# Performance work log

Hardware: AMD Instinct MI355X
Metric: run time of the kernel (lower is better)

The kernel has to match this reference:

```python
import jax, jax.numpy as jnp
import numpy as np

B, T, N, K = 8, 1024, 64, 8


def _normalize_logprob(logmat, axis):
    # temperature = 1 in forward_backward
    norm = jax.scipy.special.logsumexp(logmat, axis=axis, keepdims=True)
    return logmat - norm, norm


def setup_inputs() -> dict:
    key = jax.random.key(0)
    k1, k2, k3 = jax.random.split(key, 3)
    log_a = jax.random.normal(k1, (B, T, N, K, K), dtype=jnp.float32)
    log_b = jax.random.normal(k2, (B, T, N, K), dtype=jnp.float32)
    logprob_z1 = jax.random.normal(k3, (N, K), dtype=jnp.float32)
    return {"log_a": log_a, "log_b": log_b, "logprob_z1": logprob_z1}


def reference(log_a, log_b, logprob_z1):
    # log_a: (B,T,N,K,K)  transition log-probs a[t][i,j] = p(z_t=i | z_{t-1}=j)
    # log_b: (B,T,N,K)    emission log-likelihoods
    # logprob_z1: (N,K)   initial state log-prob (Z_init parameter)
    b_tm = jnp.moveaxis(log_b, 1, 0)  # (T,B,N,K) time-major for scan
    a_tm = jnp.moveaxis(log_a, 1, 0)  # (T,B,N,K,K)

    # ---- forward recursion ----
    alpha0, norm0 = _normalize_logprob(logprob_z1[None] + log_b[:, 0], -1)  # (B,N,K),(B,N,1)

    def fstep(prev, xs):
        b_t, a_t = xs  # (B,N,K), (B,N,K,K)
        # alpha_t[i] = logsumexp_j( b_t[i] + a_t[i,j] + prev[j] )
        u = jax.scipy.special.logsumexp(
            b_t[..., :, None] + a_t + prev[..., None, :], axis=-1)
        alpha, nrm = _normalize_logprob(u, -1)
        return alpha, (alpha, nrm)

    _, (alphas, fnorms) = jax.lax.scan(fstep, alpha0, (b_tm[1:], a_tm[1:]))
    forward_probs = jnp.moveaxis(
        jnp.concatenate([alpha0[None], alphas], axis=0), 0, 1)  # (B,T,N,K)

    # ---- backward recursion ----
    betaT = jnp.zeros_like(alpha0)  # (B,N,K)

    def bstep(nxt, xs):
        b_tp1, a_tp1 = xs  # (B,N,K), (B,N,K,K)
        # beta_t[j] = logsumexp_i( nxt[i] + a_tp1[i,j] + b_tp1[i] )
        u = jax.scipy.special.logsumexp(
            nxt[..., :, None] + a_tp1 + b_tp1[..., :, None], axis=-2)
        beta, nrm = _normalize_logprob(u, -1)
        return beta, (beta, nrm)

    _, (betas, bnorms) = jax.lax.scan(
        bstep, betaT, (b_tm[1:], a_tm[1:]), reverse=True)
    backward_probs = jnp.moveaxis(
        jnp.concatenate([betas, betaT[None]], axis=0), 0, 1)  # (B,T,N,K)

    # ---- posteriors ----
    gamma1, _ = _normalize_logprob(forward_probs + backward_probs, -1)  # (B,T,N,K)

    # gamma2[t][i,j] ~ beta_t[i] + a_t[i,j] + b_t[i] + alpha_{t-1}[j], t >= 1
    g2u = (forward_probs[:, :-1, :, None, :]      # (B,T-1,N,1,K)
           + backward_probs[:, 1:, :, :, None]    # (B,T-1,N,K,1)
           + log_a[:, 1:]                         # (B,T-1,N,K,K)
           + log_b[:, 1:][..., None])             # (B,T-1,N,K,1)
    g2_norm = jax.scipy.special.logsumexp(g2u, axis=(-2, -1), keepdims=True)
    gamma2_unpad = g2u - g2_norm
    gamma2 = jnp.concatenate(
        [jnp.zeros_like(gamma2_unpad[:, :1]), gamma2_unpad], axis=1)  # (B,T,N,K,K)

    return forward_probs, backward_probs, gamma1, gamma2
```

## Files before the change

kernel.cpp:

```cpp
#include <hip/hip_runtime.h>

#define Tdim 1024
#define Ndim 64
#define FSZ (8 * 1024 * 64 * 8)

typedef unsigned uint2v __attribute__((ext_vector_type(2)));

#define DPPADD(v, ctrl) ((v) + __int_as_float(__builtin_amdgcn_update_dpp( \
    0, __float_as_int(v), ctrl, 0xF, 0xF, false)))

__device__ __forceinline__ float swap_add16(float v) {
  unsigned u = __float_as_uint(v);
  uint2v r = __builtin_amdgcn_permlane16_swap(u, u, false, false);
  return __uint_as_float(r[0]) + __uint_as_float(r[1]);
}
__device__ __forceinline__ float swap_add32(float v) {
  unsigned u = __float_as_uint(v);
  uint2v r = __builtin_amdgcn_permlane32_swap(u, u, false, false);
  return __uint_as_float(r[0]) + __uint_as_float(r[1]);
}

#define SUM_LO3(v) { v = DPPADD(v, 0xB1); v = DPPADD(v, 0x4E); v = DPPADD(v, 0x141); }
#define SUM_HI3(v) { v = DPPADD(v, 0x128); v = swap_add16(v); v = swap_add32(v); }


__device__ __forceinline__ void fwd_load(const float* __restrict__ a_base,
                                         const float* __restrict__ b_base,
                                         int t0, int lane, int tr, int x, int y,
                                         float (&ra)[16], float (&rb)[16]) {
#pragma unroll
  for (int s = 0; s < 16; ++s) {
    int t = t0 + s; if (t > Tdim - 1) t = Tdim - 1;
    ra[s] = a_base[(size_t)t * (Ndim * 64) + ((s & 1) ? tr : lane)];
    rb[s] = b_base[(size_t)t * (Ndim * 8) + ((s & 1) ? y : x)];
  }
}

__device__ __forceinline__ void fwd_compute(int t0, int x, int y,
                                            const float (&ra)[16], const float (&rb)[16],
                                            float& q, float& sc,
                                            float* __restrict__ f_base) {
#pragma unroll
  for (int s = 0; s < 16; ++s) {
    int t = t0 + s;
    if (t < Tdim) {
      int oidx = (s & 1) ? y : x;
      float v = __expf(ra[s]) * q;
      if (!(s & 1)) { SUM_LO3(v); } else { SUM_HI3(v); }
      float S = v * (__expf(rb[s]) * sc);
      q = S;
      float T = S;
      if (!(s & 1)) { SUM_HI3(T); } else { SUM_LO3(T); }
      sc = __builtin_amdgcn_rcpf(T);
      float la = __logf(S * sc);
      if ((((s & 1) ? x : y)) == 0) f_base[(size_t)t * (Ndim * 8) + oidx] = la;
    }
  }
}

__device__ __forceinline__ void bwd_load(const float* __restrict__ a_base,
                                         const float* __restrict__ b_base,
                                         int t0, int lane, int tr, int x, int y,
                                         float (&ra)[16], float (&rb)[16]) {
#pragma unroll
  for (int s = 0; s < 16; ++s) {
    int t = t0 - s; if (t < 0) t = 0;
    ra[s] = a_base[(size_t)t * (Ndim * 64) + ((s & 1) ? tr : lane)];
    int tb = t0 - 1 - s; if (tb < 0) tb = 0;
    rb[s] = b_base[(size_t)tb * (Ndim * 8) + ((s & 1) ? x : y)];
  }
}

__device__ __forceinline__ void bwd_compute(int t0, int x, int y,
                                            const float (&ra)[16], const float (&rb)[16],
                                            float& u, float& sc,
                                            float* __restrict__ bo) {
#pragma unroll
  for (int s = 0; s < 16; ++s) {
    int tau = t0 - s;
    if (tau >= 1) {
      float v = __expf(ra[s]) * u;
      if (!(s & 1)) { SUM_HI3(v); } else { SUM_LO3(v); }
      int oidx = (s & 1) ? x : y;
      float unew = (__expf(rb[s]) * sc) * v;
      float W = v;
      if (!(s & 1)) { SUM_LO3(W); } else { SUM_HI3(W); }
      float scn = __builtin_amdgcn_rcpf(W);
      float lb = __logf(v * scn);
      if ((((s & 1) ? y : x)) == 0) bo[(size_t)(tau - 1) * (Ndim * 8) + oidx] = lb;
      u = unew;
      sc = scn;
    }
  }
}

__global__ __launch_bounds__(64, 1) void chains_kernel(const float* __restrict__ A,
                                                       const float* __restrict__ Bm,
                                                       const float* __restrict__ Z1,
                                                       float* __restrict__ Fout,
                                                       float* __restrict__ Bout) {
  const int lane = threadIdx.x;
  const int x = lane >> 3, y = lane & 7;
  const int tr = (y << 3) | x;
  const int chain = blockIdx.x & 511;
  const int b = chain >> 6, n = chain & 63;
  const size_t cbase = ((size_t)b * Tdim) * Ndim + n;
  const float* a_base = A + cbase * 64;
  const float* b_base = Bm + cbase * 8;

  float ra0[16], ra1[16], rb0[16], rb1[16];

  if (blockIdx.x < 512) {
    float* f_base = Fout + cbase * 8;
    float v0 = Z1[n * 8 + y] + b_base[y];
    float q = __expf(v0);
    float T0 = q; SUM_LO3(T0);
    if (x == 0) f_base[y] = v0 - __logf(T0);
    float sc = __builtin_amdgcn_rcpf(T0);
    fwd_load(a_base, b_base, 1, lane, tr, x, y, ra0, rb0);
#pragma unroll 1
    for (int kk = 0; kk < 64; kk += 2) {
      fwd_load(a_base, b_base, 1 + (kk + 1) * 16, lane, tr, x, y, ra1, rb1);
      __builtin_amdgcn_sched_barrier(0);
      fwd_compute(1 + kk * 16, x, y, ra0, rb0, q, sc, f_base);
      if (kk + 2 < 64) fwd_load(a_base, b_base, 1 + (kk + 2) * 16, lane, tr, x, y, ra0, rb0);
      __builtin_amdgcn_sched_barrier(0);
      fwd_compute(1 + (kk + 1) * 16, x, y, ra1, rb1, q, sc, f_base);
    }
  } else {
    float* bo = Bout + cbase * 8;
    float bT = b_base[(size_t)(Tdim - 1) * (Ndim * 8) + x];
    float u = __expf(bT);
    if (x == 0) bo[(size_t)(Tdim - 1) * (Ndim * 8) + y] = 0.f;
    float sc = 1.0f;
    bwd_load(a_base, b_base, Tdim - 1, lane, tr, x, y, ra0, rb0);
#pragma unroll 1
    for (int kk = 0; kk < 64; kk += 2) {
      bwd_load(a_base, b_base, Tdim - 1 - (kk + 1) * 16, lane, tr, x, y, ra1, rb1);
      __builtin_amdgcn_sched_barrier(0);
      bwd_compute(Tdim - 1 - kk * 16, x, y, ra0, rb0, u, sc, bo);
      if (kk + 2 < 64) bwd_load(a_base, b_base, Tdim - 1 - (kk + 2) * 16, lane, tr, x, y, ra0, rb0);
      __builtin_amdgcn_sched_barrier(0);
      bwd_compute(Tdim - 1 - (kk + 1) * 16, x, y, ra1, rb1, u, sc, bo);
    }
  }
}

__global__ __launch_bounds__(256) void gamma_kernel(const float* __restrict__ A,
                                                    const float* __restrict__ Bm,
                                                    const float* __restrict__ F,
                                                    const float* __restrict__ Bo,
                                                    float* __restrict__ G1,
                                                    float* __restrict__ G2) {
  const int lane = threadIdx.x & 63;
  const int i = lane & 7;
  const int gq = lane >> 3;
  const int g = (blockIdx.x * 4 + (threadIdx.x >> 6)) * 8 + gq;
  const int t = (g >> 6) & (Tdim - 1);

  const float bo_i = Bo[(size_t)g * 8 + i];

  {
    float u1 = F[(size_t)g * 8 + i] + bo_i;
    float s1 = __expf(u1);
    SUM_LO3(s1);
    G1[(size_t)g * 8 + i] = u1 - __logf(s1);
  }

  float4* o = (float4*)&G2[(size_t)g * 64 + i * 8];
  if (t == 0) {
    float4 z = make_float4(0.f, 0.f, 0.f, 0.f);
    o[0] = z; o[1] = z;
  } else {
    const float4* ap = (const float4*)&A[(size_t)g * 64 + i * 8];
    float4 a0 = ap[0], a1 = ap[1];
    const float4* fp = (const float4*)&F[((size_t)g - Ndim) * 8];
    float4 f0 = fp[0], f1 = fp[1];
    float c = bo_i + Bm[(size_t)g * 8 + i];
    float v0 = c + a0.x + f0.x, v1 = c + a0.y + f0.y;
    float v2 = c + a0.z + f0.z, v3 = c + a0.w + f0.w;
    float v4 = c + a1.x + f1.x, v5 = c + a1.y + f1.y;
    float v6 = c + a1.z + f1.z, v7 = c + a1.w + f1.w;
    float r = ((__expf(v0) + __expf(v1)) + (__expf(v2) + __expf(v3)))
            + ((__expf(v4) + __expf(v5)) + (__expf(v6) + __expf(v7)));
    SUM_LO3(r);
    float lq = __logf(r);
    o[0] = make_float4(v0 - lq, v1 - lq, v2 - lq, v3 - lq);
    o[1] = make_float4(v4 - lq, v5 - lq, v6 - lq, v7 - lq);
  }
}

extern "C" void kernel_launch(void* const* d_in, const int* in_sizes, int n_in,
                              void* d_out, int out_size, void* d_ws, size_t ws_size,
                              hipStream_t stream) {
  const float* A  = (const float*)d_in[0];
  const float* Bm = (const float*)d_in[1];
  const float* Z1 = (const float*)d_in[2];
  float* out = (float*)d_out;
  float* Fout = out;
  float* Bout = out + FSZ;
  float* G1   = out + 2 * FSZ;
  float* G2   = out + 3 * FSZ;

  chains_kernel<<<dim3(1024), dim3(64), 0, stream>>>(A, Bm, Z1, Fout, Bout);
  gamma_kernel<<<dim3(8 * Tdim * Ndim / 32), dim3(256), 0, stream>>>(A, Bm, Fout, Bout, G1, G2);
}
```

Before: 463.8 us.

## Stage chain transition and emission tiles into LDS via direct global-to-LDS loads

The forward and backward recursion kernels no longer prefetch 16 timesteps of transition and emission values into large register arrays. Instead they issue global_load_lds DMA loads into double-buffered shared-memory tiles, using an XOR swizzle so the transposed odd-step reads avoid bank conflicts. The compute loops then read from LDS with a small four-deep rotating register prefetch. The aim is to cut register pressure and instruction overhead on the serial, latency-bound chain. In exchange it adds LDS read latency on the critical path and relies on correct wait-count handling for the LDS DMA writes, since only lgkmcnt is waited on explicitly.

Result: faster. 451.8 us (-2.6%).

```diff
diff --git a/kernel.cpp b/kernel.cpp
--- a/kernel.cpp
+++ b/kernel.cpp
@@ -23,31 +23,69 @@
 #define SUM_LO3(v) { v = DPPADD(v, 0xB1); v = DPPADD(v, 0x4E); v = DPPADD(v, 0x141); }
 #define SUM_HI3(v) { v = DPPADD(v, 0x128); v = swap_add16(v); v = swap_add32(v); }
 
-
-__device__ __forceinline__ void fwd_load(const float* __restrict__ a_base,
-                                         const float* __restrict__ b_base,
-                                         int t0, int lane, int tr, int x, int y,
-                                         float (&ra)[16], float (&rb)[16]) {
+#define GLOAD_LDS(gp, lp) __builtin_amdgcn_global_load_lds( \
+    (const __attribute__((address_space(1))) unsigned*)(gp), \
+    (__attribute__((address_space(3))) unsigned*)(lp), 4, 0, 0)
+
+
+__device__ __forceinline__ void stage_fwd(const float* __restrict__ a_base,
+                                          const float* __restrict__ b_base,
+                                          int t0, int swz, int lane,
+                                          float* sA, float* sB) {
+  asm volatile("s_waitcnt lgkmcnt(0)" ::: "memory");
 #pragma unroll
   for (int s = 0; s < 16; ++s) {
     int t = t0 + s; if (t > Tdim - 1) t = Tdim - 1;
-    ra[s] = a_base[(size_t)t * (Ndim * 64) + ((s & 1) ? tr : lane)];
-    rb[s] = b_base[(size_t)t * (Ndim * 8) + ((s & 1) ? y : x)];
-  }
-}
-
-__device__ __forceinline__ void fwd_compute(int t0, int x, int y,
-                                            const float (&ra)[16], const float (&rb)[16],
-                                            float& q, float& sc,
-                                            float* __restrict__ f_base) {
+    GLOAD_LDS(&a_base[(size_t)t * (Ndim * 64) + swz], &sA[s * 64]);
+  }
+#pragma unroll
+  for (int h = 0; h < 2; ++h) {
+    int tb = t0 + h * 8 + (lane >> 3); if (tb > Tdim - 1) tb = Tdim - 1;
+    GLOAD_LDS(&b_base[(size_t)tb * (Ndim * 8) + (lane & 7)], &sB[h * 64]);
+  }
+}
+
+__device__ __forceinline__ void stage_bwd(const float* __restrict__ a_base,
+                                          const float* __restrict__ b_base,
+                                          int t0, int swz, int lane,
+                                          float* sA, float* sB) {
+  asm volatile("s_waitcnt lgkmcnt(0)" ::: "memory");
+#pragma unroll
+  for (int s = 0; s < 16; ++s) {
+    int t = t0 - s; if (t < 0) t = 0;
+    GLOAD_LDS(&a_base[(size_t)t * (Ndim * 64) + swz], &sA[s * 64]);
+  }
+#pragma unroll
+  for (int h = 0; h < 2; ++h) {
+    int tb = t0 - 1 - (h * 8 + (lane >> 3)); if (tb < 0) tb = 0;
+    GLOAD_LDS(&b_base[(size_t)tb * (Ndim * 8) + (lane & 7)], &sB[h * 64]);
+  }
+}
+
+__device__ __forceinline__ void fwd_compute_lds(int t0, int x, int y, int swz, int trw,
+                                                const float* sA, const float* sB,
+                                                float& q, float& sc,
+                                                float* __restrict__ f_base) {
+  float av[4], bv[4];
+#pragma unroll
+  for (int p = 0; p < 4; ++p) {
+    av[p] = sA[p * 64 + ((p & 1) ? trw : swz)];
+    bv[p] = sB[p * 8 + ((p & 1) ? y : x)];
+  }
 #pragma unroll
   for (int s = 0; s < 16; ++s) {
     int t = t0 + s;
+    float a = av[s & 3], bb = bv[s & 3];
+    if (s + 4 < 16) {
+      int p = s + 4;
+      av[s & 3] = sA[p * 64 + ((p & 1) ? trw : swz)];
+      bv[s & 3] = sB[p * 8 + ((p & 1) ? y : x)];
+    }
     if (t < Tdim) {
       int oidx = (s & 1) ? y : x;
-      float v = __expf(ra[s]) * q;
+      float v = __expf(a) * q;
       if (!(s & 1)) { SUM_LO3(v); } else { SUM_HI3(v); }
-      float S = v * (__expf(rb[s]) * sc);
+      float S = v * (__expf(bb) * sc);
       q = S;
       float T = S;
       if (!(s & 1)) { SUM_HI3(T); } else { SUM_LO3(T); }
@@ -58,31 +96,30 @@
   }
 }
 
-__device__ __forceinline__ void bwd_load(const float* __restrict__ a_base,
-                                         const float* __restrict__ b_base,
-                                         int t0, int lane, int tr, int x, int y,
-                                         float (&ra)[16], float (&rb)[16]) {
-#pragma unroll
-  for (int s = 0; s < 16; ++s) {
-    int t = t0 - s; if (t < 0) t = 0;
-    ra[s] = a_base[(size_t)t * (Ndim * 64) + ((s & 1) ? tr : lane)];
-    int tb = t0 - 1 - s; if (tb < 0) tb = 0;
-    rb[s] = b_base[(size_t)tb * (Ndim * 8) + ((s & 1) ? x : y)];
-  }
-}
-
-__device__ __forceinline__ void bwd_compute(int t0, int x, int y,
-                                            const float (&ra)[16], const float (&rb)[16],
-                                            float& u, float& sc,
-                                            float* __restrict__ bo) {
+__device__ __forceinline__ void bwd_compute_lds(int t0, int x, int y, int swz, int trw,
+                                                const float* sA, const float* sB,
+                                                float& u, float& sc,
+                                                float* __restrict__ bo) {
+  float av[4], bv[4];
+#pragma unroll
+  for (int p = 0; p < 4; ++p) {
+    av[p] = sA[p * 64 + ((p & 1) ? trw : swz)];
+    bv[p] = sB[p * 8 + ((p & 1) ? x : y)];
+  }
 #pragma unroll
   for (int s = 0; s < 16; ++s) {
     int tau = t0 - s;
+    float a = av[s & 3], bb = bv[s & 3];
+    if (s + 4 < 16) {
+      int p = s + 4;
+      av[s & 3] = sA[p * 64 + ((p & 1) ? trw : swz)];
+      bv[s & 3] = sB[p * 8 + ((p & 1) ? x : y)];
+    }
     if (tau >= 1) {
-      float v = __expf(ra[s]) * u;
+      float v = __expf(a) * u;
       if (!(s & 1)) { SUM_HI3(v); } else { SUM_LO3(v); }
       int oidx = (s & 1) ? x : y;
-      float unew = (__expf(rb[s]) * sc) * v;
+      float unew = (__expf(bb) * sc) * v;
       float W = v;
       if (!(s & 1)) { SUM_LO3(W); } else { SUM_HI3(W); }
       float scn = __builtin_amdgcn_rcpf(W);
@@ -99,16 +136,16 @@
                                                        const float* __restrict__ Z1,
                                                        float* __restrict__ Fout,
                                                        float* __restrict__ Bout) {
+  __shared__ float sA0[1024], sA1[1024], sB0[128], sB1[128];
   const int lane = threadIdx.x;
   const int x = lane >> 3, y = lane & 7;
-  const int tr = (y << 3) | x;
+  const int swz = (x << 3) | (y ^ x);
+  const int trw = (y << 3) | (x ^ y);
   const int chain = blockIdx.x & 511;
   const int b = chain >> 6, n = chain & 63;
   const size_t cbase = ((size_t)b * Tdim) * Ndim + n;
   const float* a_base = A + cbase * 64;
   const float* b_base = Bm + cbase * 8;
-
-  float ra0[16], ra1[16], rb0[16], rb1[16];
 
   if (blockIdx.x < 512) {
     float* f_base = Fout + cbase * 8;
@@ -117,15 +154,13 @@
     float T0 = q; SUM_LO3(T0);
     if (x == 0) f_base[y] = v0 - __logf(T0);
     float sc = __builtin_amdgcn_rcpf(T0);
-    fwd_load(a_base, b_base, 1, lane, tr, x, y, ra0, rb0);
+    stage_fwd(a_base, b_base, 1, swz, lane, sA0, sB0);
 #pragma unroll 1
     for (int kk = 0; kk < 64; kk += 2) {
-      fwd_load(a_base, b_base, 1 + (kk + 1) * 16, lane, tr, x, y, ra1, rb1);
-      __builtin_amdgcn_sched_barrier(0);
-      fwd_compute(1 + kk * 16, x, y, ra0, rb0, q, sc, f_base);
-      if (kk + 2 < 64) fwd_load(a_base, b_base, 1 + (kk + 2) * 16, lane, tr, x, y, ra0, rb0);
-      __builtin_amdgcn_sched_barrier(0);
-      fwd_compute(1 + (kk + 1) * 16, x, y, ra1, rb1, q, sc, f_base);
+      stage_fwd(a_base, b_base, 1 + (kk + 1) * 16, swz, lane, sA1, sB1);
+      fwd_compute_lds(1 + kk * 16, x, y, swz, trw, sA0, sB0, q, sc, f_base);
+      if (kk + 2 < 64) stage_fwd(a_base, b_base, 1 + (kk + 2) * 16, swz, lane, sA0, sB0);
+      fwd_compute_lds(1 + (kk + 1) * 16, x, y, swz, trw, sA1, sB1, q, sc, f_base);
     }
   } else {
     float* bo = Bout + cbase * 8;
@@ -133,15 +168,13 @@
     float u = __expf(bT);
     if (x == 0) bo[(size_t)(Tdim - 1) * (Ndim * 8) + y] = 0.f;
     float sc = 1.0f;
-    bwd_load(a_base, b_base, Tdim - 1, lane, tr, x, y, ra0, rb0);
+    stage_bwd(a_base, b_base, Tdim - 1, swz, lane, sA0, sB0);
 #pragma unroll 1
     for (int kk = 0; kk < 64; kk += 2) {
-      bwd_load(a_base, b_base, Tdim - 1 - (kk + 1) * 16, lane, tr, x, y, ra1, rb1);
-      __builtin_amdgcn_sched_barrier(0);
-      bwd_compute(Tdim - 1 - kk * 16, x, y, ra0, rb0, u, sc, bo);
-      if (kk + 2 < 64) bwd_load(a_base, b_base, Tdim - 1 - (kk + 2) * 16, lane, tr, x, y, ra0, rb0);
-      __builtin_amdgcn_sched_barrier(0);
-      bwd_compute(Tdim - 1 - (kk + 1) * 16, x, y, ra1, rb1, u, sc, bo);
+      stage_bwd(a_base, b_base, Tdim - 1 - (kk + 1) * 16, swz, lane, sA1, sB1);
+      bwd_compute_lds(Tdim - 1 - kk * 16, x, y, swz, trw, sA0, sB0, u, sc, bo);
+      if (kk + 2 < 64) stage_bwd(a_base, b_base, Tdim - 1 - (kk + 2) * 16, swz, lane, sA0, sB0);
+      bwd_compute_lds(Tdim - 1 - (kk + 1) * 16, x, y, swz, trw, sA1, sB1, u, sc, bo);
     }
   }
 }
```
